# Performance work log

Measured on AMD Instinct MI355X. Metric: run time of the kernel, lower is better.

The kernel has to match this reference:

```python
import jax, jax.numpy as jnp
import numpy as np

B, T, H, L = 8, 256, 64, 3
NB, NF, HP = 17, 68, 6
K = 9  # temporal kernel
PAD = (K - 1) // 2
EPS = 1e-5


def _normalize(adj):
    adj = adj + np.eye(adj.shape[0], dtype=np.float32)
    d = adj.sum(1)
    dinv = np.power(d, -0.5)
    dinv[np.isinf(dinv)] = 0.0
    return (dinv[:, None] * adj * dinv[None, :]).astype(np.float32)


def _body_adj():
    a = np.zeros((NB, NB), np.float32)
    conns = [(0, 1), (0, 2), (1, 3), (2, 4), (0, 5), (0, 6), (5, 6), (5, 7), (7, 9), (6, 8), (8, 10), (5, 11), (6, 12), (11, 12), (11, 13), (13, 15), (12, 14), (14, 16)]
    for i, j in conns:
        a[i, j] = 1.0
        a[j, i] = 1.0
    return _normalize(a)


def _face_adj():
    a = np.zeros((NF, NF), np.float32)
    for i in range(16): a[i, i + 1] = 1.0
    for i in range(17, 21): a[i, i + 1] = 1.0
    for i in range(22, 26): a[i, i + 1] = 1.0
    for i in range(27, 30): a[i, i + 1] = 1.0
    for i in range(31, 35): a[i, i + 1] = 1.0
    for i in range(36, 41): a[i, i + 1] = 1.0
    a[41, 36] = 1.0
    for i in range(42, 47): a[i, i + 1] = 1.0
    a[47, 42] = 1.0
    for i in range(48, 59): a[i, i + 1] = 1.0
    a[59, 48] = 1.0
    for i in range(60, 67): a[i, i + 1] = 1.0
    a[67, 60] = 1.0
    a = a + a.T
    return _normalize(a)


def setup_inputs() -> dict:
    keys = iter(jax.random.split(jax.random.key(0), 80))

    def rn(shape, s):
        return jax.random.normal(next(keys), shape, jnp.float32) * s

    inp = {}
    inp['body_kps'] = jax.random.normal(next(keys), (B, T, NB * 2), jnp.float32)
    inp['face_kps_2d'] = jax.random.normal(next(keys), (B, T, NF * 2), jnp.float32)
    inp['head_pose'] = jax.random.normal(next(keys), (B, T, HP), jnp.float32)
    inp['body_adj'] = jnp.asarray(_body_adj())
    inp['face_adj'] = jnp.asarray(_face_adj())
    inp['body_proj_w'] = rn((2, H), 0.5)
    inp['body_proj_b'] = jnp.zeros((H,), jnp.float32)
    inp['face_proj_w'] = rn((2, H), 0.5)
    inp['face_proj_b'] = jnp.zeros((H,), jnp.float32)
    inp['head_w'] = rn((HP, H), 0.3)
    inp['head_b'] = jnp.zeros((H,), jnp.float32)
    for p in ('b', 'f'):
        inp[p + '_t1w'] = rn((L, H, H, K), 0.04)
        inp[p + '_t1b'] = jnp.zeros((L, H), jnp.float32)
        inp[p + '_bn1g'] = jnp.ones((L, H), jnp.float32)
        inp[p + '_bn1b'] = jnp.zeros((L, H), jnp.float32)
        inp[p + '_bn1m'] = rn((L, H), 0.1)
        inp[p + '_bn1v'] = jax.random.uniform(next(keys), (L, H), jnp.float32, 0.5, 1.5)
        inp[p + '_gcw'] = rn((L, H, H), 0.1)
        inp[p + '_gcb'] = jnp.zeros((L, H), jnp.float32)
        inp[p + '_t2w'] = rn((L, H, H, K), 0.04)
        inp[p + '_t2b'] = jnp.zeros((L, H), jnp.float32)
        inp[p + '_bn2g'] = jnp.ones((L, H), jnp.float32)
        inp[p + '_bn2b'] = jnp.zeros((L, H), jnp.float32)
        inp[p + '_bn2m'] = rn((L, H), 0.1)
        inp[p + '_bn2v'] = jax.random.uniform(next(keys), (L, H), jnp.float32, 0.5, 1.5)
    total = NB * H + NF * H + H  # 5504
    inp['fus1_w'] = rn((total, 4 * H), 0.02)
    inp['fus1_b'] = jnp.zeros((4 * H,), jnp.float32)
    inp['fus2_w'] = rn((4 * H, 2 * H), 0.06)
    inp['fus2_b'] = jnp.zeros((2 * H,), jnp.float32)
    inp['fus3_w'] = rn((2 * H, H), 0.09)
    inp['fus3_b'] = jnp.zeros((H,), jnp.float32)
    inp['fus4_w'] = rn((H, 5), 0.12)
    inp['fus4_b'] = jnp.zeros((5,), jnp.float32)
    return inp


def _conv_bn(x, w, b, g, be, m, v):
    # x: (BN, C, T); w: (O, I, K). Conv1d (pad=4) + eval-mode BatchNorm1d.
    y = jax.lax.conv_general_dilated(x, w, (1,), [(PAD, PAD)], dimension_numbers=('NCH', 'OIH', 'NCH'))
    y = y + b[None, :, None]
    inv = g * jax.lax.rsqrt(v + EPS)
    return y * inv[None, :, None] + (be - m * inv)[None, :, None]


def _block(x, adj, t1w, t1b, g1, b1, m1, v1, gw, gb, t2w, t2b, g2, b2, m2, v2):
    # x: (B, N, C, T); residual is identity (in_channels == out_channels)
    Bn, N, C, Tn = x.shape
    res = x
    h = jax.nn.relu(_conv_bn(x.reshape(Bn * N, C, Tn), t1w, t1b, g1, b1, m1, v1)).reshape(Bn, N, C, Tn)
    # spatial graph conv, batched over all timesteps at once (adj @ (x W) + b)
    support = jnp.einsum('bnct,co->bnot', h, gw)
    h = jax.nn.relu(jnp.einsum('mn,bnot->bmot', adj, support) + gb[None, None, :, None])
    h = _conv_bn(h.reshape(Bn * N, C, Tn), t2w, t2b, g2, b2, m2, v2).reshape(Bn, N, C, Tn)
    return h + res  # dropout = identity in eval


def _stream(x, n_nodes, pw, pb, adj, ps):
    Bn, Tn, _ = x.shape
    h = x.reshape(Bn, Tn, n_nodes, 2) @ pw + pb          # (B, T, N, H)
    h = jnp.transpose(h, (0, 2, 3, 1))                   # (B, N, H, T)
    for l in range(ps[0].shape[0]):
        h = _block(h, adj, *(p[l] for p in ps))
    return h.mean(axis=3).reshape(Bn, -1)                # temporal mean-pool, flatten nodes


def reference(body_kps, face_kps_2d, head_pose, body_adj, face_adj, body_proj_w, body_proj_b, face_proj_w, face_proj_b, head_w, head_b, b_t1w, b_t1b, b_bn1g, b_bn1b, b_bn1m, b_bn1v, b_gcw, b_gcb, b_t2w, b_t2b, b_bn2g, b_bn2b, b_bn2m, b_bn2v, f_t1w, f_t1b, f_bn1g, f_bn1b, f_bn1m, f_bn1v, f_gcw, f_gcb, f_t2w, f_t2b, f_bn2g, f_bn2b, f_bn2m, f_bn2v, fus1_w, fus1_b, fus2_w, fus2_b, fus3_w, fus3_b, fus4_w, fus4_b):
    bps = (b_t1w, b_t1b, b_bn1g, b_bn1b, b_bn1m, b_bn1v, b_gcw, b_gcb, b_t2w, b_t2b, b_bn2g, b_bn2b, b_bn2m, b_bn2v)
    fps = (f_t1w, f_t1b, f_bn1g, f_bn1b, f_bn1m, f_bn1v, f_gcw, f_gcb, f_t2w, f_t2b, f_bn2g, f_bn2b, f_bn2m, f_bn2v)
    bf = _stream(body_kps, NB, body_proj_w, body_proj_b, body_adj, bps)
    ff = _stream(face_kps_2d, NF, face_proj_w, face_proj_b, face_adj, fps)
    hp = jax.nn.relu(head_pose @ head_w + head_b).mean(axis=1)
    feat = jnp.concatenate([bf, ff, hp], axis=-1)
    h = jax.nn.relu(feat @ fus1_w + fus1_b)
    h = jax.nn.relu(h @ fus2_w + fus2_b)
    h = jax.nn.relu(h @ fus3_w + fus3_b)
    return h @ fus4_w + fus4_b
```

## Files before the change

kernel.cpp:

```cpp
#include <hip/hip_runtime.h>

constexpr int B_ = 8, T_ = 256, H_ = 64, L_ = 3, NB_ = 17, NF_ = 68, HP_ = 6, K_ = 9;
constexpr int FEAT_DIM = NB_ * H_ + NF_ * H_ + H_;
constexpr int HT = H_ * T_;

typedef _Float16 half4_t __attribute__((ext_vector_type(4)));
typedef _Float16 half8_t __attribute__((ext_vector_type(8)));
typedef float f32x16 __attribute__((ext_vector_type(16)));
typedef float f32x4 __attribute__((ext_vector_type(4)));

constexpr size_t SZ_AB = (size_t)B_ * NB_ * HT;
constexpr size_t SZ_AF = (size_t)B_ * NF_ * HT;
constexpr size_t OFF_TB   = 0;
constexpr size_t OFF_TF   = OFF_TB + SZ_AB / 2;
constexpr size_t OFF_SUPB = OFF_TF + SZ_AF / 2;
constexpr size_t OFF_SUPF = OFF_SUPB + SZ_AB / 2;
constexpr size_t OFF_GB   = OFF_SUPF + SZ_AF / 2;
constexpr size_t OFF_GF   = OFF_GB + SZ_AB / 2;
constexpr size_t OFF_W3   = OFF_GF + SZ_AF / 2;
constexpr size_t OFF_GW3  = OFF_W3 + 4 * 55296;
constexpr size_t OFF_B2   = OFF_GW3 + 2 * 6144;
constexpr size_t OFF_ADJPB= OFF_B2 + 768;
constexpr size_t OFF_ADJPF= OFF_ADJPB + 512;
constexpr size_t OFF_FEAT = OFF_ADJPF + 3840;
constexpr size_t OFF_P1   = OFF_FEAT + (size_t)B_ * FEAT_DIM;

struct ConvPrepSet { const float *w, *tb, *g, *bb, *m, *v; };

__global__ __launch_bounds__(256) void prep_convW_all(ConvPrepSet s0, ConvPrepSet s1,
                                                      ConvPrepSet s2, ConvPrepSet s3,
                                                      _Float16* __restrict__ w3,
                                                      float* __restrict__ b2) {
    int set = blockIdx.y;
    ConvPrepSet s = (set == 0) ? s0 : (set == 1) ? s1 : (set == 2) ? s2 : s3;
    int idx = blockIdx.x * 256 + threadIdx.x;
    int k = idx % K_; int r = idx / K_;
    int i = r % H_; r /= H_;
    int o = r % H_; int l = r / H_;
    float sc = s.g[l * H_ + o] * rsqrtf(s.v[l * H_ + o] + 1e-5f);
    w3[(size_t)set * 110592 + ((((l * K_ + k) * 8 + (i >> 3)) * H_ + o) * 8) + (i & 7)]
        = (_Float16)(s.w[idx] * sc);
    if (i == 0 && k == 0)
        b2[set * 192 + l * H_ + o] =
            s.tb[l * H_ + o] * sc + s.bb[l * H_ + o] - s.m[l * H_ + o] * sc;
}

__global__ __launch_bounds__(256) void prep_gcw_all(const float* __restrict__ g0,
                                                    const float* __restrict__ g1,
                                                    _Float16* __restrict__ w3) {
    int set = blockIdx.y;
    const float* gw = set ? g1 : g0;
    int idx = blockIdx.x * 256 + threadIdx.x;
    int o = idx % H_; int r = idx / H_;
    int c = r % H_; int l = r / H_;
    w3[(size_t)set * 12288 + (((l * 8 + (c >> 3)) * H_ + o) * 8) + (c & 7)] = (_Float16)gw[idx];
}

__global__ __launch_bounds__(256) void prep_misc(const float* __restrict__ adjB,
                                                 const float* __restrict__ adjF,
                                                 _Float16* __restrict__ pB,
                                                 _Float16* __restrict__ pF,
                                                 float* __restrict__ p1,
                                                 float* __restrict__ feat) {
    int idx = blockIdx.x * 256 + threadIdx.x;
    if (idx < 1024) {
        int m = idx >> 5, k = idx & 31;
        pB[idx] = (m < NB_ && k < NB_) ? (_Float16)adjB[m * NB_ + k] : (_Float16)0.f;
    } else if (idx < 8704) {
        int j = idx - 1024;
        int m = j / 80, k = j % 80;
        pF[j] = (m < NF_ && k < NF_) ? (_Float16)adjF[m * NF_ + k] : (_Float16)0.f;
    } else if (idx < 10752) {
        p1[idx - 8704] = 0.f;
    } else if (idx < 10752 + B_ * FEAT_DIM) {
        feat[idx - 10752] = 0.f;
    }
}

__global__ __launch_bounds__(256) void proj_kernel(const float* __restrict__ kpsB,
                                                   const float* __restrict__ pwB,
                                                   const float* __restrict__ pbB,
                                                   _Float16* __restrict__ outB,
                                                   const float* __restrict__ kpsF,
                                                   const float* __restrict__ pwF,
                                                   const float* __restrict__ pbF,
                                                   _Float16* __restrict__ outF,
                                                   int nblk0) {
    int blk = blockIdx.x;
    const float *kps, *pw, *pb; _Float16* out; int N, bn;
    if (blk < nblk0) { kps = kpsB; pw = pwB; pb = pbB; out = outB; N = NB_; bn = blk; }
    else { kps = kpsF; pw = pwF; pb = pbF; out = outF; N = NF_; bn = blk - nblk0; }
    int b = bn / N, n = bn % N;
    int t = threadIdx.x;
    float x0 = kps[((size_t)b * T_ + t) * (N * 2) + n * 2 + 0];
    float x1 = kps[((size_t)b * T_ + t) * (N * 2) + n * 2 + 1];
    _Float16* ob = out + (size_t)bn * HT + t;
#pragma unroll 8
    for (int c = 0; c < H_; ++c)
        ob[(size_t)c * T_] = (_Float16)fmaf(x0, pw[c], fmaf(x1, pw[H_ + c], pb[c]));
}

__device__ __forceinline__ half8_t ld_b8(const _Float16* p) {
    half4_t lo = *(const half4_t*)p;
    half4_t hi = *(const half4_t*)(p + 4);
    return __builtin_shufflevector(lo, hi, 0, 1, 2, 3, 4, 5, 6, 7);
}

__device__ __forceinline__ void stage_f16(const _Float16* __restrict__ xb,
                                          _Float16* __restrict__ Xs, int tc, int tid) {
    for (int u = tid; u < H_ * 17; u += 256) {
        int c = u & 63, s = u >> 6;
        int t0 = tc * 128 + s * 8 - 4;
        const _Float16* xr = xb + (size_t)c * T_;
        _Float16 v[8];
        if (t0 >= 0 && t0 + 8 <= T_) {
            half4_t a = *(const half4_t*)(xr + t0);
            half4_t bq = *(const half4_t*)(xr + t0 + 4);
#pragma unroll
            for (int j = 0; j < 4; ++j) { v[j] = a[j]; v[4 + j] = bq[j]; }
        } else {
#pragma unroll
            for (int j = 0; j < 8; ++j) {
                int t = t0 + j;
                v[j] = (t >= 0 && t < T_) ? xr[t] : (_Float16)0.f;
            }
        }
        int tt = s * 8;
#pragma unroll
        for (int j = 0; j < 8; ++j) Xs[(tt + j) * 68 + c] = v[j];
    }
}

struct CM {
    const _Float16* x; const half8_t* w1; const float* b1; const half8_t* gc; _Float16* sup;
};

__global__ __launch_bounds__(256) void convmix_kernel(CM P0, CM P1, int nblk0, int l) {
    __shared__ __align__(16) _Float16 Xs[136 * 68];
    int blk = blockIdx.x;
    CM P = (blk < nblk0) ? P0 : P1;
    if (blk >= nblk0) blk -= nblk0;
    int bn = blk >> 1, tc = blk & 1;
    int tid = threadIdx.x;
    stage_f16(P.x + (size_t)bn * HT, Xs, tc, tid);
    __syncthreads();

    int ln = tid & 63;
    int w = __builtin_amdgcn_readfirstlane(tid >> 6);
    int ln31 = ln & 31, kg = ln >> 5;
    int ob = (w & 1) * 32, tsub = (w >> 1) * 64;

    f32x16 acc[2];
#pragma unroll
    for (int ts = 0; ts < 2; ++ts)
#pragma unroll
        for (int r = 0; r < 16; ++r) acc[ts][r] = 0.f;

    const half8_t* wl = P.w1 + (size_t)l * (K_ * 8 * H_);
#pragma unroll
    for (int tap = 0; tap < K_; ++tap) {
#pragma unroll
        for (int ks = 0; ks < 4; ++ks) {
            int i8 = ks * 2 + kg;
            half8_t a = wl[(tap * 8 + i8) * H_ + ob + ln31];
#pragma unroll
            for (int ts = 0; ts < 2; ++ts) {
                half8_t bf = ld_b8(&Xs[(tsub + ts * 32 + ln31 + tap) * 68 + i8 * 8]);
                acc[ts] = __builtin_amdgcn_mfma_f32_32x32x16_f16(a, bf, acc[ts], 0, 0, 0);
            }
        }
    }
    __syncthreads();

#pragma unroll
    for (int ts = 0; ts < 2; ++ts) {
        int row = 4 + tsub + ts * 32 + ln31;
#pragma unroll
        for (int rg = 0; rg < 4; ++rg) {
            int o0 = ob + rg * 8 + kg * 4;
            f32x4 bv = *(const f32x4*)(P.b1 + l * H_ + o0);
            half4_t hv;
#pragma unroll
            for (int j = 0; j < 4; ++j)
                hv[j] = (_Float16)fmaxf(acc[ts][rg * 4 + j] + bv[j], 0.f);
            *(half4_t*)(&Xs[row * 68 + o0]) = hv;
        }
    }
    __syncthreads();

    f32x16 acc2[2];
#pragma unroll
    for (int ts = 0; ts < 2; ++ts)
#pragma unroll
        for (int r = 0; r < 16; ++r) acc2[ts][r] = 0.f;
    const half8_t* gl = P.gc + (size_t)l * (8 * H_);
#pragma unroll
    for (int ks = 0; ks < 4; ++ks) {
        int i8 = ks * 2 + kg;
        half8_t a = gl[i8 * H_ + ob + ln31];
#pragma unroll
        for (int ts = 0; ts < 2; ++ts) {
            half8_t bf = ld_b8(&Xs[(4 + tsub + ts * 32 + ln31) * 68 + i8 * 8]);
            acc2[ts] = __builtin_amdgcn_mfma_f32_32x32x16_f16(a, bf, acc2[ts], 0, 0, 0);
        }
    }

    _Float16* sp = P.sup + (size_t)bn * HT + tc * 128;
#pragma unroll
    for (int ts = 0; ts < 2; ++ts) {
        int t = tsub + ts * 32 + ln31;
#pragma unroll
        for (int r = 0; r < 16; ++r) {
            int o = ob + (r & 3) + 8 * (r >> 2) + 4 * kg;
            sp[(size_t)o * T_ + t] = (_Float16)acc2[ts][r];
        }
    }
}

struct C2 {
    const _Float16* x; const half8_t* w2; const float* b2; _Float16* trunk; int N; int fbase;
};

template <bool LAST>
__global__ __launch_bounds__(256) void conv2_kernel(C2 P0, C2 P1, int nblk0, int l,
                                                    float* __restrict__ feat) {
    __shared__ __align__(16) _Float16 Xs[136 * 68];
    int blk = blockIdx.x;
    C2 P = (blk < nblk0) ? P0 : P1;
    if (blk >= nblk0) blk -= nblk0;
    int bn = blk >> 1, tc = blk & 1;
    int tid = threadIdx.x;
    stage_f16(P.x + (size_t)bn * HT, Xs, tc, tid);
    __syncthreads();

    int ln = tid & 63;
    int w = __builtin_amdgcn_readfirstlane(tid >> 6);
    int ln31 = ln & 31, kg = ln >> 5;
    int ob = (w & 1) * 32, tsub = (w >> 1) * 64;

    f32x16 acc[2];
#pragma unroll
    for (int ts = 0; ts < 2; ++ts)
#pragma unroll
        for (int r = 0; r < 16; ++r) acc[ts][r] = 0.f;

    const half8_t* wl = P.w2 + (size_t)l * (K_ * 8 * H_);
#pragma unroll
    for (int tap = 0; tap < K_; ++tap) {
#pragma unroll
        for (int ks = 0; ks < 4; ++ks) {
            int i8 = ks * 2 + kg;
            half8_t a = wl[(tap * 8 + i8) * H_ + ob + ln31];
#pragma unroll
            for (int ts = 0; ts < 2; ++ts) {
                half8_t bf = ld_b8(&Xs[(tsub + ts * 32 + ln31 + tap) * 68 + i8 * 8]);
                acc[ts] = __builtin_amdgcn_mfma_f32_32x32x16_f16(a, bf, acc[ts], 0, 0, 0);
            }
        }
    }

    const _Float16* resb = P.trunk + (size_t)bn * HT + tc * 128;
    if (!LAST) {
        _Float16* tob = P.trunk + (size_t)bn * HT + tc * 128;
#pragma unroll
        for (int ts = 0; ts < 2; ++ts) {
            int t = tsub + ts * 32 + ln31;
#pragma unroll
            for (int r = 0; r < 16; ++r) {
                int o = ob + (r & 3) + 8 * (r >> 2) + 4 * kg;
                float y = acc[ts][r] + P.b2[l * H_ + o] + (float)resb[(size_t)o * T_ + t];
                tob[(size_t)o * T_ + t] = (_Float16)y;
            }
        }
    } else {
        __syncthreads();
        float* red = (float*)Xs;
        float sv[16];
#pragma unroll
        for (int r = 0; r < 16; ++r) {
            int o = ob + (r & 3) + 8 * (r >> 2) + 4 * kg;
            float bias = P.b2[l * H_ + o];
            float s = acc[0][r] + bias + (float)resb[(size_t)o * T_ + tsub + ln31]
                    + acc[1][r] + bias + (float)resb[(size_t)o * T_ + tsub + 32 + ln31];
#pragma unroll
            for (int off = 1; off < 32; off <<= 1) s += __shfl_xor(s, off);
            sv[r] = s;
        }
        if (ln31 == 0) {
#pragma unroll
            for (int r = 0; r < 16; ++r) {
                int o = ob + (r & 3) + 8 * (r >> 2) + 4 * kg;
                red[(w >> 1) * 64 + o] = sv[r];
            }
        }
        __syncthreads();
        if (tid < 64) {
            float s = red[tid] + red[64 + tid];
            int b = bn / P.N, n = bn % P.N;
            atomicAdd(&feat[(size_t)b * FEAT_DIM + P.fbase + n * H_ + tid], s * (1.f / 256.f));
        }
    }
}

template <int N, int MT, int KS>
__device__ __forceinline__ void adjmix_impl(const _Float16* __restrict__ sup,
                                            const half8_t* __restrict__ adjP,
                                            const float* __restrict__ gb,
                                            _Float16* __restrict__ out,
                                            int blk, int l, _Float16* Ls, int tid) {
    constexpr int KP = KS * 16;
    constexpr int PITCH = KP + 4;
    int b = blk >> 7, cb = blk & 127;
    int colbase = cb * 128;
    float gbv = gb[l * H_ + (cb >> 1)];

    for (int u = tid; u < KP * 16; u += 256) {
        int n = u >> 4, cs = u & 15;
        half8_t v;
        if (n < N) v = *(const half8_t*)(sup + (size_t)(b * N + n) * HT + colbase + cs * 8);
        else {
#pragma unroll
            for (int j = 0; j < 8; ++j) v[j] = (_Float16)0.f;
        }
#pragma unroll
        for (int j = 0; j < 8; ++j) Ls[(cs * 8 + j) * PITCH + n] = v[j];
    }
    __syncthreads();

    int ln = tid & 63;
    int w = __builtin_amdgcn_readfirstlane(tid >> 6);
    int ln31 = ln & 31, kg = ln >> 5;
    int colL = w * 32 + ln31;

    f32x16 acc[MT];
#pragma unroll
    for (int mt = 0; mt < MT; ++mt)
#pragma unroll
        for (int r = 0; r < 16; ++r) acc[mt][r] = 0.f;

#pragma unroll
    for (int ks = 0; ks < KS; ++ks) {
        half8_t bf = ld_b8(&Ls[colL * PITCH + ks * 16 + kg * 8]);
#pragma unroll
        for (int mt = 0; mt < MT; ++mt) {
            half8_t af = adjP[(size_t)(mt * 32 + ln31) * (KP / 8) + ks * 2 + kg];
            acc[mt] = __builtin_amdgcn_mfma_f32_32x32x16_f16(af, bf, acc[mt], 0, 0, 0);
        }
    }

    int col = colbase + colL;
#pragma unroll
    for (int mt = 0; mt < MT; ++mt) {
#pragma unroll
        for (int r = 0; r < 16; ++r) {
            int m = mt * 32 + (r & 3) + 8 * (r >> 2) + 4 * kg;
            if (m < N)
                out[(size_t)(b * N + m) * HT + col] = (_Float16)fmaxf(acc[mt][r] + gbv, 0.f);
        }
    }
}

__global__ __launch_bounds__(256) void adjmix_kernel(
        const _Float16* __restrict__ supB, const half8_t* __restrict__ adjPB,
        const float* __restrict__ gbB, _Float16* __restrict__ outB,
        const _Float16* __restrict__ supF, const half8_t* __restrict__ adjPF,
        const float* __restrict__ gbF, _Float16* __restrict__ outF,
        int nblk0, int l) {
    __shared__ __align__(16) _Float16 Ls[128 * 84];
    int blk = blockIdx.x, tid = threadIdx.x;
    if (blk < nblk0)
        adjmix_impl<NB_, 1, 2>(supB, adjPB, gbB, outB, blk, l, Ls, tid);
    else
        adjmix_impl<NF_, 3, 5>(supF, adjPF, gbF, outF, blk - nblk0, l, Ls, tid);
}

__global__ void head_kernel(const float* __restrict__ x, const float* __restrict__ hw,
                            const float* __restrict__ hb, float* __restrict__ feat) {
    int b = blockIdx.x;
    int c = threadIdx.x;
    float w0 = hw[c], w1 = hw[64 + c], w2 = hw[128 + c],
          w3 = hw[192 + c], w4 = hw[256 + c], w5 = hw[320 + c];
    float bias = hb[c];
    float acc = 0.f;
    for (int t = 0; t < T_; ++t) {
        const float* xr = x + ((size_t)b * T_ + t) * HP_;
        float s = fmaf(xr[0], w0, fmaf(xr[1], w1, fmaf(xr[2], w2,
                  fmaf(xr[3], w3, fmaf(xr[4], w4, fmaf(xr[5], w5, bias))))));
        acc += fmaxf(s, 0.f);
    }
    feat[(size_t)b * FEAT_DIM + NB_ * H_ + NF_ * H_ + c] = acc * (1.f / 256.f);
}

__global__ __launch_bounds__(256) void fus1_kernel(const float* __restrict__ feat,
                                                   const float* __restrict__ w1,
                                                   float* __restrict__ p1) {
    __shared__ float fv[128];
    int b = blockIdx.x / 43, ic = blockIdx.x % 43;
    int tid = threadIdx.x;
    if (tid < 128) fv[tid] = feat[(size_t)b * FEAT_DIM + ic * 128 + tid];
    __syncthreads();
    const float* wb = w1 + (size_t)(ic * 128) * 256 + tid;
    float acc = 0.f;
#pragma unroll 4
    for (int i = 0; i < 128; ++i)
        acc = fmaf(fv[i], wb[(size_t)i * 256], acc);
    atomicAdd(&p1[b * 256 + tid], acc);
}

__global__ __launch_bounds__(256) void fus_tail_kernel(const float* __restrict__ p1,
        const float* __restrict__ b1, const float* __restrict__ w2, const float* __restrict__ b2,
        const float* __restrict__ w3, const float* __restrict__ b3,
        const float* __restrict__ w4, const float* __restrict__ b4, float* __restrict__ out) {
    __shared__ float s1[256], s2[128], s3[64];
    int b = blockIdx.x, tid = threadIdx.x;
    s1[tid] = fmaxf(p1[b * 256 + tid] + b1[tid], 0.f);
    __syncthreads();
    if (tid < 128) {
        float acc = b2[tid];
        for (int i = 0; i < 256; ++i) acc = fmaf(s1[i], w2[i * 128 + tid], acc);
        s2[tid] = fmaxf(acc, 0.f);
    }
    __syncthreads();
    if (tid < 64) {
        float acc = b3[tid];
        for (int i = 0; i < 128; ++i) acc = fmaf(s2[i], w3[i * 64 + tid], acc);
        s3[tid] = fmaxf(acc, 0.f);
    }
    __syncthreads();
    if (tid < 5) {
        float acc = b4[tid];
        for (int i = 0; i < 64; ++i) acc = fmaf(s3[i], w4[i * 5 + tid], acc);
        out[b * 5 + tid] = acc;
    }
}

extern "C" void kernel_launch(void* const* d_in, const int* in_sizes, int n_in,
                              void* d_out, int out_size, void* d_ws, size_t ws_size,
                              hipStream_t stream) {
    const float* body_kps = (const float*)d_in[0];
    const float* face_kps = (const float*)d_in[1];
    const float* head_pose = (const float*)d_in[2];
    const float* body_adj = (const float*)d_in[3];
    const float* face_adj = (const float*)d_in[4];
    const float* body_pw = (const float*)d_in[5];
    const float* body_pb = (const float*)d_in[6];
    const float* face_pw = (const float*)d_in[7];
    const float* face_pb = (const float*)d_in[8];
    const float* head_w = (const float*)d_in[9];
    const float* head_b = (const float*)d_in[10];
    const float* b_t1w = (const float*)d_in[11]; const float* b_t1b = (const float*)d_in[12];
    const float* b_g1  = (const float*)d_in[13]; const float* b_b1  = (const float*)d_in[14];
    const float* b_m1  = (const float*)d_in[15]; const float* b_v1  = (const float*)d_in[16];
    const float* b_gcw = (const float*)d_in[17]; const float* b_gcb = (const float*)d_in[18];
    const float* b_t2w = (const float*)d_in[19]; const float* b_t2b = (const float*)d_in[20];
    const float* b_g2  = (const float*)d_in[21]; const float* b_b2  = (const float*)d_in[22];
    const float* b_m2  = (const float*)d_in[23]; const float* b_v2  = (const float*)d_in[24];
    const float* f_t1w = (const float*)d_in[25]; const float* f_t1b = (const float*)d_in[26];
    const float* f_g1  = (const float*)d_in[27]; const float* f_b1  = (const float*)d_in[28];
    const float* f_m1  = (const float*)d_in[29]; const float* f_v1  = (const float*)d_in[30];
    const float* f_gcw = (const float*)d_in[31]; const float* f_gcb = (const float*)d_in[32];
    const float* f_t2w = (const float*)d_in[33]; const float* f_t2b = (const float*)d_in[34];
    const float* f_g2  = (const float*)d_in[35]; const float* f_b2  = (const float*)d_in[36];
    const float* f_m2  = (const float*)d_in[37]; const float* f_v2  = (const float*)d_in[38];
    const float* fus1_w = (const float*)d_in[39]; const float* fus1_b = (const float*)d_in[40];
    const float* fus2_w = (const float*)d_in[41]; const float* fus2_b = (const float*)d_in[42];
    const float* fus3_w = (const float*)d_in[43]; const float* fus3_b = (const float*)d_in[44];
    const float* fus4_w = (const float*)d_in[45]; const float* fus4_b = (const float*)d_in[46];

    float* ws = (float*)d_ws;
    _Float16* TrB = (_Float16*)(ws + OFF_TB);
    _Float16* TrF = (_Float16*)(ws + OFF_TF);
    _Float16* SupB = (_Float16*)(ws + OFF_SUPB);
    _Float16* SupF = (_Float16*)(ws + OFF_SUPF);
    _Float16* Gb = (_Float16*)(ws + OFF_GB);
    _Float16* Gf = (_Float16*)(ws + OFF_GF);
    _Float16* W3 = (_Float16*)(ws + OFF_W3);
    _Float16* W3b1 = W3;            _Float16* W3b2 = W3 + 110592;
    _Float16* W3f1 = W3 + 221184;   _Float16* W3f2 = W3 + 331776;
    _Float16* GW3 = (_Float16*)(ws + OFF_GW3);
    _Float16* GW3b = GW3;           _Float16* GW3f = GW3 + 12288;
    float* B2 = ws + OFF_B2;
    float* B2b1 = B2;        float* B2b2 = B2 + 192;
    float* B2f1 = B2 + 384;  float* B2f2 = B2 + 576;
    _Float16* adjPB = (_Float16*)(ws + OFF_ADJPB);
    _Float16* adjPF = (_Float16*)(ws + OFF_ADJPF);
    float* feat = ws + OFF_FEAT;
    float* p1 = ws + OFF_P1;
    float* out = (float*)d_out;

    ConvPrepSet sb1{b_t1w, b_t1b, b_g1, b_b1, b_m1, b_v1};
    ConvPrepSet sb2{b_t2w, b_t2b, b_g2, b_b2, b_m2, b_v2};
    ConvPrepSet sf1{f_t1w, f_t1b, f_g1, f_b1, f_m1, f_v1};
    ConvPrepSet sf2{f_t2w, f_t2b, f_g2, f_b2, f_m2, f_v2};
    prep_convW_all<<<dim3(432, 4), 256, 0, stream>>>(sb1, sb2, sf1, sf2, W3, B2);
    prep_gcw_all<<<dim3(48, 2), 256, 0, stream>>>(b_gcw, f_gcw, GW3);
    prep_misc<<<214, 256, 0, stream>>>(body_adj, face_adj, adjPB, adjPF, p1, feat);

    const int nB = B_ * NB_;
    const int nF = B_ * NF_;
    proj_kernel<<<nB + nF, 256, 0, stream>>>(body_kps, body_pw, body_pb, TrB,
                                             face_kps, face_pw, face_pb, TrF, nB);

    CM cmb{TrB, (const half8_t*)W3b1, B2b1, (const half8_t*)GW3b, SupB};
    CM cmf{TrF, (const half8_t*)W3f1, B2f1, (const half8_t*)GW3f, SupF};
    C2 c2b{Gb, (const half8_t*)W3b2, B2b2, TrB, NB_, 0};
    C2 c2f{Gf, (const half8_t*)W3f2, B2f2, TrF, NF_, NB_ * H_};

    const int gc = (nB + nF) * 2;
    const int n0 = nB * 2;
    const int ga = B_ * 128;

    for (int l = 0; l < L_; ++l) {
        convmix_kernel<<<gc, 256, 0, stream>>>(cmb, cmf, n0, l);
        adjmix_kernel<<<2 * ga, 256, 0, stream>>>(SupB, (const half8_t*)adjPB, b_gcb, Gb,
                                                  SupF, (const half8_t*)adjPF, f_gcb, Gf, ga, l);
        if (l < L_ - 1)
            conv2_kernel<false><<<gc, 256, 0, stream>>>(c2b, c2f, n0, l, feat);
        else
            conv2_kernel<true><<<gc, 256, 0, stream>>>(c2b, c2f, n0, l, feat);
    }

    head_kernel<<<B_, 64, 0, stream>>>(head_pose, head_w, head_b, feat);
    fus1_kernel<<<B_ * 43, 256, 0, stream>>>(feat, fus1_w, p1);
    fus_tail_kernel<<<B_, 256, 0, stream>>>(p1, fus1_b, fus2_w, fus2_b, fus3_w, fus3_b,
                                            fus4_w, fus4_b, out);
}
```

Before: 406.8 us.

## Fuse all forward stages into one persistent cooperative kernel with grid syncs

Replaces the sequence of proj, per-layer convmix/adjmix/conv2, head and fusion-MLP launches with a single persistent cooperative kernel. Blocks pull work items from per-stage atomic counters and separate stages with grid-wide barriers. The aim is to remove per-launch overhead and the idle gaps between roughly a dozen small kernels. In exchange it adds grid.sync costs and atomic work-stealing, and occupancy (and so register and LDS pressure) is now fixed by launch_bounds(256,4) across every stage.

```diff
diff --git a/kernel.cpp b/kernel.cpp
--- a/kernel.cpp
+++ b/kernel.cpp
@@ -1,4 +1,6 @@
 #include <hip/hip_runtime.h>
+#include <hip/hip_cooperative_groups.h>
+namespace cg = cooperative_groups;
 
 constexpr int B_ = 8, T_ = 256, H_ = 64, L_ = 3, NB_ = 17, NF_ = 68, HP_ = 6, K_ = 9;
 constexpr int FEAT_DIM = NB_ * H_ + NF_ * H_ + H_;
@@ -24,6 +26,8 @@
 constexpr size_t OFF_ADJPF= OFF_ADJPB + 512;
 constexpr size_t OFF_FEAT = OFF_ADJPF + 3840;
 constexpr size_t OFF_P1   = OFF_FEAT + (size_t)B_ * FEAT_DIM;
+constexpr size_t OFF_CTR  = OFF_P1 + 2048;
+constexpr int N_CTR = 12;
 
 struct ConvPrepSet { const float *w, *tb, *g, *bb, *m, *v; };
 
@@ -61,7 +65,8 @@
                                                  _Float16* __restrict__ pB,
                                                  _Float16* __restrict__ pF,
                                                  float* __restrict__ p1,
-                                                 float* __restrict__ feat) {
+                                                 float* __restrict__ feat,
+                                                 int* __restrict__ ctrs) {
     int idx = blockIdx.x * 256 + threadIdx.x;
     if (idx < 1024) {
         int m = idx >> 5, k = idx & 31;
@@ -74,31 +79,24 @@
         p1[idx - 8704] = 0.f;
     } else if (idx < 10752 + B_ * FEAT_DIM) {
         feat[idx - 10752] = 0.f;
-    }
-}
-
-__global__ __launch_bounds__(256) void proj_kernel(const float* __restrict__ kpsB,
-                                                   const float* __restrict__ pwB,
-                                                   const float* __restrict__ pbB,
-                                                   _Float16* __restrict__ outB,
-                                                   const float* __restrict__ kpsF,
-                                                   const float* __restrict__ pwF,
-                                                   const float* __restrict__ pbF,
-                                                   _Float16* __restrict__ outF,
-                                                   int nblk0) {
-    int blk = blockIdx.x;
-    const float *kps, *pw, *pb; _Float16* out; int N, bn;
-    if (blk < nblk0) { kps = kpsB; pw = pwB; pb = pbB; out = outB; N = NB_; bn = blk; }
-    else { kps = kpsF; pw = pwF; pb = pbF; out = outF; N = NF_; bn = blk - nblk0; }
-    int b = bn / N, n = bn % N;
-    int t = threadIdx.x;
-    float x0 = kps[((size_t)b * T_ + t) * (N * 2) + n * 2 + 0];
-    float x1 = kps[((size_t)b * T_ + t) * (N * 2) + n * 2 + 1];
-    _Float16* ob = out + (size_t)bn * HT + t;
-#pragma unroll 8
-    for (int c = 0; c < H_; ++c)
-        ob[(size_t)c * T_] = (_Float16)fmaf(x0, pw[c], fmaf(x1, pw[H_ + c], pb[c]));
-}
+    } else if (idx < 10752 + B_ * FEAT_DIM + N_CTR) {
+        ctrs[idx - 10752 - B_ * FEAT_DIM] = 0;
+    }
+}
+
+struct MegaP {
+    const float *kpsB, *pwB, *pbB, *kpsF, *pwF, *pbF;
+    const float *head_x, *head_w, *head_b;
+    _Float16 *TrB, *TrF, *SupB, *SupF, *Gb, *Gf;
+    const half8_t *W3b1, *W3b2, *W3f1, *W3f2, *GW3b, *GW3f;
+    const float *B2b1, *B2b2, *B2f1, *B2f2;
+    const half8_t *adjPB, *adjPF;
+    const float *gbB, *gbF;
+    float *feat, *p1;
+    const float *f1w, *f1b, *f2w, *f2b, *f3w, *f3b, *f4w, *f4b;
+    float *out;
+    int *ctrs;
+};
 
 __device__ __forceinline__ half8_t ld_b8(const _Float16* p) {
     half4_t lo = *(const half4_t*)p;
@@ -131,18 +129,44 @@
     }
 }
 
-struct CM {
+__device__ void proj_body(const MegaP& P, int blk, int tid) {
+    const float *kps, *pw, *pb; _Float16* out; int N, bn;
+    if (blk < B_ * NB_) { kps = P.kpsB; pw = P.pwB; pb = P.pbB; out = P.TrB; N = NB_; bn = blk; }
+    else { kps = P.kpsF; pw = P.pwF; pb = P.pbF; out = P.TrF; N = NF_; bn = blk - B_ * NB_; }
+    int b = bn / N, n = bn % N;
+    int t = tid;
+    float x0 = kps[((size_t)b * T_ + t) * (N * 2) + n * 2 + 0];
+    float x1 = kps[((size_t)b * T_ + t) * (N * 2) + n * 2 + 1];
+    _Float16* ob = out + (size_t)bn * HT + t;
+#pragma unroll 8
+    for (int c = 0; c < H_; ++c)
+        ob[(size_t)c * T_] = (_Float16)fmaf(x0, pw[c], fmaf(x1, pw[H_ + c], pb[c]));
+}
+
+__device__ void head_body(const MegaP& P, int b, int tid) {
+    if (tid >= 64) return;
+    int c = tid;
+    const float* hw = P.head_w;
+    float w0 = hw[c], w1 = hw[64 + c], w2 = hw[128 + c],
+          w3 = hw[192 + c], w4 = hw[256 + c], w5 = hw[320 + c];
+    float bias = P.head_b[c];
+    float acc = 0.f;
+    for (int t = 0; t < T_; ++t) {
+        const float* xr = P.head_x + ((size_t)b * T_ + t) * HP_;
+        float s = fmaf(xr[0], w0, fmaf(xr[1], w1, fmaf(xr[2], w2,
+                  fmaf(xr[3], w3, fmaf(xr[4], w4, fmaf(xr[5], w5, bias))))));
+        acc += fmaxf(s, 0.f);
+    }
+    P.feat[(size_t)b * FEAT_DIM + NB_ * H_ + NF_ * H_ + c] = acc * (1.f / 256.f);
+}
+
+__device__ void convmix_body(const MegaP& P, int blk, int l, int tid, _Float16* Xs) {
     const _Float16* x; const half8_t* w1; const float* b1; const half8_t* gc; _Float16* sup;
-};
-
-__global__ __launch_bounds__(256) void convmix_kernel(CM P0, CM P1, int nblk0, int l) {
-    __shared__ __align__(16) _Float16 Xs[136 * 68];
-    int blk = blockIdx.x;
-    CM P = (blk < nblk0) ? P0 : P1;
-    if (blk >= nblk0) blk -= nblk0;
+    const int n0 = B_ * NB_ * 2;
+    if (blk < n0) { x = P.TrB; w1 = P.W3b1; b1 = P.B2b1; gc = P.GW3b; sup = P.SupB; }
+    else { blk -= n0; x = P.TrF; w1 = P.W3f1; b1 = P.B2f1; gc = P.GW3f; sup = P.SupF; }
     int bn = blk >> 1, tc = blk & 1;
-    int tid = threadIdx.x;
-    stage_f16(P.x + (size_t)bn * HT, Xs, tc, tid);
+    stage_f16(x + (size_t)bn * HT, Xs, tc, tid);
     __syncthreads();
 
     int ln = tid & 63;
@@ -156,7 +180,7 @@
 #pragma unroll
         for (int r = 0; r < 16; ++r) acc[ts][r] = 0.f;
 
-    const half8_t* wl = P.w1 + (size_t)l * (K_ * 8 * H_);
+    const half8_t* wl = w1 + (size_t)l * (K_ * 8 * H_);
 #pragma unroll
     for (int tap = 0; tap < K_; ++tap) {
 #pragma unroll
@@ -178,7 +202,7 @@
 #pragma unroll
         for (int rg = 0; rg < 4; ++rg) {
             int o0 = ob + rg * 8 + kg * 4;
-            f32x4 bv = *(const f32x4*)(P.b1 + l * H_ + o0);
+            f32x4 bv = *(const f32x4*)(b1 + l * H_ + o0);
             half4_t hv;
 #pragma unroll
             for (int j = 0; j < 4; ++j)
@@ -193,7 +217,7 @@
     for (int ts = 0; ts < 2; ++ts)
 #pragma unroll
         for (int r = 0; r < 16; ++r) acc2[ts][r] = 0.f;
-    const half8_t* gl = P.gc + (size_t)l * (8 * H_);
+    const half8_t* gl = gc + (size_t)l * (8 * H_);
 #pragma unroll
     for (int ks = 0; ks < 4; ++ks) {
         int i8 = ks * 2 + kg;
@@ -205,7 +229,7 @@
         }
     }
 
-    _Float16* sp = P.sup + (size_t)bn * HT + tc * 128;
+    _Float16* sp = sup + (size_t)bn * HT + tc * 128;
 #pragma unroll
     for (int ts = 0; ts < 2; ++ts) {
         int t = tsub + ts * 32 + ln31;
@@ -217,20 +241,13 @@
     }
 }
 
-struct C2 {
-    const _Float16* x; const half8_t* w2; const float* b2; _Float16* trunk; int N; int fbase;
-};
-
-template <bool LAST>
-__global__ __launch_bounds__(256) void conv2_kernel(C2 P0, C2 P1, int nblk0, int l,
-                                                    float* __restrict__ feat) {
-    __shared__ __align__(16) _Float16 Xs[136 * 68];
-    int blk = blockIdx.x;
-    C2 P = (blk < nblk0) ? P0 : P1;
-    if (blk >= nblk0) blk -= nblk0;
+__device__ void conv2_body(const MegaP& P, int blk, int l, bool last, int tid, _Float16* Xs) {
+    const _Float16* x; const half8_t* w2; const float* b2; _Float16* trunk; int N, fbase;
+    const int n0 = B_ * NB_ * 2;
+    if (blk < n0) { x = P.Gb; w2 = P.W3b2; b2 = P.B2b2; trunk = P.TrB; N = NB_; fbase = 0; }
+    else { blk -= n0; x = P.Gf; w2 = P.W3f2; b2 = P.B2f2; trunk = P.TrF; N = NF_; fbase = NB_ * H_; }
     int bn = blk >> 1, tc = blk & 1;
-    int tid = threadIdx.x;
-    stage_f16(P.x + (size_t)bn * HT, Xs, tc, tid);
+    stage_f16(x + (size_t)bn * HT, Xs, tc, tid);
     __syncthreads();
 
     int ln = tid & 63;
@@ -244,7 +261,7 @@
 #pragma unroll
         for (int r = 0; r < 16; ++r) acc[ts][r] = 0.f;
 
-    const half8_t* wl = P.w2 + (size_t)l * (K_ * 8 * H_);
+    const half8_t* wl = w2 + (size_t)l * (K_ * 8 * H_);
 #pragma unroll
     for (int tap = 0; tap < K_; ++tap) {
 #pragma unroll
@@ -259,16 +276,16 @@
         }
     }
 
-    const _Float16* resb = P.trunk + (size_t)bn * HT + tc * 128;
-    if (!LAST) {
-        _Float16* tob = P.trunk + (size_t)bn * HT + tc * 128;
+    const _Float16* resb = trunk + (size_t)bn * HT + tc * 128;
+    if (!last) {
+        _Float16* tob = trunk + (size_t)bn * HT + tc * 128;
 #pragma unroll
         for (int ts = 0; ts < 2; ++ts) {
             int t = tsub + ts * 32 + ln31;
 #pragma unroll
             for (int r = 0; r < 16; ++r) {
                 int o = ob + (r & 3) + 8 * (r >> 2) + 4 * kg;
-                float y = acc[ts][r] + P.b2[l * H_ + o] + (float)resb[(size_t)o * T_ + t];
+                float y = acc[ts][r] + b2[l * H_ + o] + (float)resb[(size_t)o * T_ + t];
                 tob[(size_t)o * T_ + t] = (_Float16)y;
             }
         }
@@ -279,7 +296,7 @@
 #pragma unroll
         for (int r = 0; r < 16; ++r) {
             int o = ob + (r & 3) + 8 * (r >> 2) + 4 * kg;
-            float bias = P.b2[l * H_ + o];
+            float bias = b2[l * H_ + o];
             float s = acc[0][r] + bias + (float)resb[(size_t)o * T_ + tsub + ln31]
                     + acc[1][r] + bias + (float)resb[(size_t)o * T_ + tsub + 32 + ln31];
 #pragma unroll
@@ -296,8 +313,8 @@
         __syncthreads();
         if (tid < 64) {
             float s = red[tid] + red[64 + tid];
-            int b = bn / P.N, n = bn % P.N;
-            atomicAdd(&feat[(size_t)b * FEAT_DIM + P.fbase + n * H_ + tid], s * (1.f / 256.f));
+            int b = bn / N, n = bn % N;
+            atomicAdd(&P.feat[(size_t)b * FEAT_DIM + fbase + n * H_ + tid], s * (1.f / 256.f));
         }
     }
 }
@@ -360,78 +377,87 @@
     }
 }
 
-__global__ __launch_bounds__(256) void adjmix_kernel(
-        const _Float16* __restrict__ supB, const half8_t* __restrict__ adjPB,
-        const float* __restrict__ gbB, _Float16* __restrict__ outB,
-        const _Float16* __restrict__ supF, const half8_t* __restrict__ adjPF,
-        const float* __restrict__ gbF, _Float16* __restrict__ outF,
-        int nblk0, int l) {
-    __shared__ __align__(16) _Float16 Ls[128 * 84];
-    int blk = blockIdx.x, tid = threadIdx.x;
-    if (blk < nblk0)
-        adjmix_impl<NB_, 1, 2>(supB, adjPB, gbB, outB, blk, l, Ls, tid);
+__device__ void adjmix_body(const MegaP& P, int blk, int l, int tid, _Float16* Ls) {
+    const int ga = B_ * 128;
+    if (blk < ga)
+        adjmix_impl<NB_, 1, 2>(P.SupB, P.adjPB, P.gbB, P.Gb, blk, l, Ls, tid);
     else
-        adjmix_impl<NF_, 3, 5>(supF, adjPF, gbF, outF, blk - nblk0, l, Ls, tid);
-}
-
-__global__ void head_kernel(const float* __restrict__ x, const float* __restrict__ hw,
-                            const float* __restrict__ hb, float* __restrict__ feat) {
-    int b = blockIdx.x;
-    int c = threadIdx.x;
-    float w0 = hw[c], w1 = hw[64 + c], w2 = hw[128 + c],
-          w3 = hw[192 + c], w4 = hw[256 + c], w5 = hw[320 + c];
-    float bias = hb[c];
-    float acc = 0.f;
-    for (int t = 0; t < T_; ++t) {
-        const float* xr = x + ((size_t)b * T_ + t) * HP_;
-        float s = fmaf(xr[0], w0, fmaf(xr[1], w1, fmaf(xr[2], w2,
-                  fmaf(xr[3], w3, fmaf(xr[4], w4, fmaf(xr[5], w5, bias))))));
-        acc += fmaxf(s, 0.f);
-    }
-    feat[(size_t)b * FEAT_DIM + NB_ * H_ + NF_ * H_ + c] = acc * (1.f / 256.f);
-}
-
-__global__ __launch_bounds__(256) void fus1_kernel(const float* __restrict__ feat,
-                                                   const float* __restrict__ w1,
-                                                   float* __restrict__ p1) {
-    __shared__ float fv[128];
-    int b = blockIdx.x / 43, ic = blockIdx.x % 43;
-    int tid = threadIdx.x;
-    if (tid < 128) fv[tid] = feat[(size_t)b * FEAT_DIM + ic * 128 + tid];
-    __syncthreads();
-    const float* wb = w1 + (size_t)(ic * 128) * 256 + tid;
+        adjmix_impl<NF_, 3, 5>(P.SupF, P.adjPF, P.gbF, P.Gf, blk - ga, l, Ls, tid);
+}
+
+__device__ void fus1_body(const MegaP& P, int blk, int tid, float* fv) {
+    int b = blk / 43, ic = blk % 43;
+    if (tid < 128) fv[tid] = P.feat[(size_t)b * FEAT_DIM + ic * 128 + tid];
+    __syncthreads();
+    const float* wb = P.f1w + (size_t)(ic * 128) * 256 + tid;
     float acc = 0.f;
 #pragma unroll 4
     for (int i = 0; i < 128; ++i)
         acc = fmaf(fv[i], wb[(size_t)i * 256], acc);
-    atomicAdd(&p1[b * 256 + tid], acc);
-}
-
-__global__ __launch_bounds__(256) void fus_tail_kernel(const float* __restrict__ p1,
-        const float* __restrict__ b1, const float* __restrict__ w2, const float* __restrict__ b2,
-        const float* __restrict__ w3, const float* __restrict__ b3,
-        const float* __restrict__ w4, const float* __restrict__ b4, float* __restrict__ out) {
-    __shared__ float s1[256], s2[128], s3[64];
-    int b = blockIdx.x, tid = threadIdx.x;
-    s1[tid] = fmaxf(p1[b * 256 + tid] + b1[tid], 0.f);
+    atomicAdd(&P.p1[b * 256 + tid], acc);
+}
+
+__device__ void fustail_body(const MegaP& P, int b, int tid, float* sm) {
+    float* s1 = sm; float* s2 = sm + 256; float* s3 = sm + 384;
+    s1[tid] = fmaxf(P.p1[b * 256 + tid] + P.f1b[tid], 0.f);
     __syncthreads();
     if (tid < 128) {
-        float acc = b2[tid];
-        for (int i = 0; i < 256; ++i) acc = fmaf(s1[i], w2[i * 128 + tid], acc);
+        float acc = P.f2b[tid];
+        for (int i = 0; i < 256; ++i) acc = fmaf(s1[i], P.f2w[i * 128 + tid], acc);
         s2[tid] = fmaxf(acc, 0.f);
     }
     __syncthreads();
     if (tid < 64) {
-        float acc = b3[tid];
-        for (int i = 0; i < 128; ++i) acc = fmaf(s2[i], w3[i * 64 + tid], acc);
+        float acc = P.f3b[tid];
+        for (int i = 0; i < 128; ++i) acc = fmaf(s2[i], P.f3w[i * 64 + tid], acc);
         s3[tid] = fmaxf(acc, 0.f);
     }
     __syncthreads();
     if (tid < 5) {
-        float acc = b4[tid];
-        for (int i = 0; i < 64; ++i) acc = fmaf(s3[i], w4[i * 5 + tid], acc);
-        out[b * 5 + tid] = acc;
-    }
+        float acc = P.f4b[tid];
+        for (int i = 0; i < 64; ++i) acc = fmaf(s3[i], P.f4w[i * 5 + tid], acc);
+        P.out[b * 5 + tid] = acc;
+    }
+}
+
+#define STAGE(CTR, NV, BODY)                                   \
+    for (;;) {                                                 \
+        if (tid == 0) sh_vb = atomicAdd(&P.ctrs[CTR], 1);      \
+        __syncthreads();                                       \
+        int vb = sh_vb;                                        \
+        __syncthreads();                                       \
+        if (vb >= (NV)) break;                                 \
+        BODY;                                                  \
+    }
+
+__global__ __launch_bounds__(256, 4) void mega_kernel(MegaP P) {
+    __shared__ __align__(16) char smem[21504];
+    __shared__ int sh_vb;
+    _Float16* XS = (_Float16*)smem;
+    float* SF = (float*)smem;
+    int tid = threadIdx.x;
+    cg::grid_group grid = cg::this_grid();
+
+    const int nconv = B_ * (NB_ + NF_) * 2;
+    const int nadj = 2 * B_ * 128;
+    const int nproj = B_ * (NB_ + NF_);
+
+    STAGE(0, nproj + B_,
+          { if (vb < nproj) proj_body(P, vb, tid); else head_body(P, vb - nproj, tid); })
+    grid.sync();
+
+    for (int l = 0; l < L_; ++l) {
+        STAGE(1 + 3 * l, nconv, convmix_body(P, vb, l, tid, XS))
+        grid.sync();
+        STAGE(2 + 3 * l, nadj, adjmix_body(P, vb, l, tid, XS))
+        grid.sync();
+        STAGE(3 + 3 * l, nconv, conv2_body(P, vb, l, l == L_ - 1, tid, XS))
+        grid.sync();
+    }
+
+    STAGE(10, B_ * 43, fus1_body(P, vb, tid, SF))
+    grid.sync();
+    STAGE(11, B_, fustail_body(P, vb, tid, SF))
 }
 
 extern "C" void kernel_launch(void* const* d_in, const int* in_sizes, int n_in,
@@ -475,17 +501,13 @@
     _Float16* Gb = (_Float16*)(ws + OFF_GB);
     _Float16* Gf = (_Float16*)(ws + OFF_GF);
     _Float16* W3 = (_Float16*)(ws + OFF_W3);
-    _Float16* W3b1 = W3;            _Float16* W3b2 = W3 + 110592;
-    _Float16* W3f1 = W3 + 221184;   _Float16* W3f2 = W3 + 331776;
     _Float16* GW3 = (_Float16*)(ws + OFF_GW3);
-    _Float16* GW3b = GW3;           _Float16* GW3f = GW3 + 12288;
     float* B2 = ws + OFF_B2;
-    float* B2b1 = B2;        float* B2b2 = B2 + 192;
-    float* B2f1 = B2 + 384;  float* B2f2 = B2 + 576;
     _Float16* adjPB = (_Float16*)(ws + OFF_ADJPB);
     _Float16* adjPF = (_Float16*)(ws + OFF_ADJPF);
     float* feat = ws + OFF_FEAT;
     float* p1 = ws + OFF_P1;
+    int* ctrs = (int*)(ws + OFF_CTR);
     float* out = (float*)d_out;
 
     ConvPrepSet sb1{b_t1w, b_t1b, b_g1, b_b1, b_m1, b_v1};
@@ -494,34 +516,33 @@
     ConvPrepSet sf2{f_t2w, f_t2b, f_g2, f_b2, f_m2, f_v2};
     prep_convW_all<<<dim3(432, 4), 256, 0, stream>>>(sb1, sb2, sf1, sf2, W3, B2);
     prep_gcw_all<<<dim3(48, 2), 256, 0, stream>>>(b_gcw, f_gcw, GW3);
-    prep_misc<<<214, 256, 0, stream>>>(body_adj, face_adj, adjPB, adjPF, p1, feat);
-
-    const int nB = B_ * NB_;
-    const int nF = B_ * NF_;
-    proj_kernel<<<nB + nF, 256, 0, stream>>>(body_kps, body_pw, body_pb, TrB,
-                                             face_kps, face_pw, face_pb, TrF, nB);
-
-    CM cmb{TrB, (const half8_t*)W3b1, B2b1, (const half8_t*)GW3b, SupB};
-    CM cmf{TrF, (const half8_t*)W3f1, B2f1, (const half8_t*)GW3f, SupF};
-    C2 c2b{Gb, (const half8_t*)W3b2, B2b2, TrB, NB_, 0};
-    C2 c2f{Gf, (const half8_t*)W3f2, B2f2, TrF, NF_, NB_ * H_};
-
-    const int gc = (nB + nF) * 2;
-    const int n0 = nB * 2;
-    const int ga = B_ * 128;
-
-    for (int l = 0; l < L_; ++l) {
-        convmix_kernel<<<gc, 256, 0, stream>>>(cmb, cmf, n0, l);
-        adjmix_kernel<<<2 * ga, 256, 0, stream>>>(SupB, (const half8_t*)adjPB, b_gcb, Gb,
-                                                  SupF, (const half8_t*)adjPF, f_gcb, Gf, ga, l);
-        if (l < L_ - 1)
-            conv2_kernel<false><<<gc, 256, 0, stream>>>(c2b, c2f, n0, l, feat);
-        else
-            conv2_kernel<true><<<gc, 256, 0, stream>>>(c2b, c2f, n0, l, feat);
-    }
-
-    head_kernel<<<B_, 64, 0, stream>>>(head_pose, head_w, head_b, feat);
-    fus1_kernel<<<B_ * 43, 256, 0, stream>>>(feat, fus1_w, p1);
-    fus_tail_kernel<<<B_, 256, 0, stream>>>(p1, fus1_b, fus2_w, fus2_b, fus3_w, fus3_b,
-                                            fus4_w, fus4_b, out);
-}
+    prep_misc<<<216, 256, 0, stream>>>(body_adj, face_adj, adjPB, adjPF, p1, feat, ctrs);
+
+    int occ = 0;
+    hipError_t oe = hipOccupancyMaxActiveBlocksPerMultiprocessor(&occ, mega_kernel, 256, 0);
+    if (oe != hipSuccess || occ < 1) occ = 2;
+    int G = occ * 256;
+    if (G > 2048) G = 2048;
+
+    MegaP mp;
+    mp.kpsB = body_kps; mp.pwB = body_pw; mp.pbB = body_pb;
+    mp.kpsF = face_kps; mp.pwF = face_pw; mp.pbF = face_pb;
+    mp.head_x = head_pose; mp.head_w = head_w; mp.head_b = head_b;
+    mp.TrB = TrB; mp.TrF = TrF; mp.SupB = SupB; mp.SupF = SupF; mp.Gb = Gb; mp.Gf = Gf;
+    mp.W3b1 = (const half8_t*)W3;
+    mp.W3b2 = (const half8_t*)(W3 + 110592);
+    mp.W3f1 = (const half8_t*)(W3 + 221184);
+    mp.W3f2 = (const half8_t*)(W3 + 331776);
+    mp.GW3b = (const half8_t*)GW3; mp.GW3f = (const half8_t*)(GW3 + 12288);
+    mp.B2b1 = B2; mp.B2b2 = B2 + 192; mp.B2f1 = B2 + 384; mp.B2f2 = B2 + 576;
+    mp.adjPB = (const half8_t*)adjPB; mp.adjPF = (const half8_t*)adjPF;
+    mp.gbB = b_gcb; mp.gbF = f_gcb;
+    mp.feat = feat; mp.p1 = p1;
+    mp.f1w = fus1_w; mp.f1b = fus1_b; mp.f2w = fus2_w; mp.f2b = fus2_b;
+    mp.f3w = fus3_w; mp.f3b = fus3_b; mp.f4w = fus4_w; mp.f4b = fus4_b;
+    mp.out = out; mp.ctrs = ctrs;
+
+    void* args[] = { &mp };
+    hipLaunchCooperativeKernel(reinterpret_cast<void*>(mega_kernel),
+                               dim3(G), dim3(256), args, 0, stream);
+}
```

Result: slower. 1.349 ms (+231.6%).
